# Kernel tuning notes

Hardware: AMD Instinct MI355X
Metric: run time of the kernel (lower is better)

The kernel has to match this reference:

```python
import jax, jax.numpy as jnp
import numpy as np

NUM_HEAD = 16
HEAD_DIM = 64
SEQ, BATCH, DMODEL = 2048, 2, 1024


def setup_inputs() -> dict:
    key = jax.random.key(0)
    ks = jax.random.split(key, 6)
    xavier = lambda k, shp: jax.random.uniform(
        k, shp, jnp.float32, -1.0, 1.0) * np.sqrt(6.0 / (shp[0] + shp[1]))
    query = jax.random.normal(ks[0], (SEQ, BATCH, DMODEL), jnp.float32)
    q_w = xavier(ks[1], (DMODEL, DMODEL))
    k_w = xavier(ks[2], (DMODEL, DMODEL))
    v_w = xavier(ks[3], (DMODEL, DMODEL))
    out_w = xavier(ks[4], (DMODEL, DMODEL))
    zeros = jnp.zeros((DMODEL,), jnp.float32)
    # causal mask: True = masked out (key position after query position)
    causal = jnp.triu(jnp.ones((SEQ, SEQ), bool), k=1)
    attn_mask = jnp.broadcast_to(causal, (BATCH, SEQ, SEQ))
    return {
        "query": query,
        "q_w": q_w, "q_b": zeros,
        "k_w": k_w, "k_b": zeros,
        "v_w": v_w, "v_b": zeros,
        "out_w": out_w, "out_b": zeros,
        "attn_mask": attn_mask,
    }


def reference(query, q_w, q_b, k_w, k_b, v_w, v_b, out_w, out_b, attn_mask):
    S, B, _ = query.shape
    H, Dh = NUM_HEAD, HEAD_DIM
    scale = 1.0 / np.sqrt(Dh)
    # self-attention: key = value = query
    q = (query @ q_w.T + q_b).reshape(S, B, H, Dh)
    k = (query @ k_w.T + k_b).reshape(S, B, H, Dh)
    v = (query @ v_w.T + v_b).reshape(S, B, H, Dh)
    # scores: [B, H, S(query), S(key)]
    scores = jnp.einsum('sbhd,tbhd->bhst', q, k) * scale
    scores = jnp.where(attn_mask[:, None, :, :], -jnp.inf, scores)
    attn = jax.nn.softmax(scores, axis=-1)
    # context: [S, B, H, Dh] -> [S, B, H*Dh]
    ctx = jnp.einsum('bhst,tbhd->sbhd', attn, v).reshape(S, B, H * Dh)
    return ctx @ out_w.T + out_b
```

## Files before the change

kernel.cpp:

```cpp
#include <hip/hip_runtime.h>
#include <hip/hip_bf16.h>

typedef __bf16 bf16;
typedef __attribute__((ext_vector_type(2))) __bf16 bf16x2;
typedef __attribute__((ext_vector_type(4))) __bf16 bf16x4;
typedef __attribute__((ext_vector_type(8))) __bf16 bf16x8;
typedef __attribute__((ext_vector_type(4))) float f32x4;

static_assert(sizeof(bf16x8) == 16, "bf16x8 must be 16B");

#define S_LEN 2048
#define BATCH_N 2
#define DM 1024
#define NHEAD 16
#define HDIM 64
#define LOG2E 1.44269504088896f

__device__ __forceinline__ void async_cp16(const void* g, void* l) {
    __builtin_amdgcn_global_load_lds(
        (const __attribute__((address_space(1))) void*)g,
        (__attribute__((address_space(3))) void*)l, 16, 0, 0);
}

__global__ __launch_bounds__(256)
void cvt_all(const float* __restrict__ q,
             const float* __restrict__ w0, const float* __restrict__ w1,
             const float* __restrict__ w2, const float* __restrict__ w3,
             bf16* __restrict__ Xb,
             bf16* __restrict__ W0, bf16* __restrict__ W1,
             bf16* __restrict__ W2, bf16* __restrict__ W3) {
    const int blk = blockIdx.x;
    const float* src;
    bf16* dst;
    size_t base;
    if (blk < 2048) {
        src = q; dst = Xb; base = (size_t)blk * 2048;
    } else {
        const int w = (blk - 2048) >> 9;
        const int r = (blk - 2048) & 511;
        base = (size_t)r * 2048;
        src = (w == 0) ? w0 : (w == 1) ? w1 : (w == 2) ? w2 : w3;
        dst = (w == 0) ? W0 : (w == 1) ? W1 : (w == 2) ? W2 : W3;
    }
    const size_t i = base + (size_t)threadIdx.x * 8;
    const f32x4 a = *(const f32x4*)(src + i);
    const f32x4 b = *(const f32x4*)(src + i + 4);
    bf16x8 r8;
    r8[0] = (bf16)a[0]; r8[1] = (bf16)a[1]; r8[2] = (bf16)a[2]; r8[3] = (bf16)a[3];
    r8[4] = (bf16)b[0]; r8[5] = (bf16)b[1]; r8[6] = (bf16)b[2]; r8[7] = (bf16)b[3];
    *(bf16x8*)(dst + i) = r8;
}

__device__ __forceinline__ void gemm_tile64(const bf16* __restrict__ A,
                                            const bf16* __restrict__ W,
                                            int row0, int col0, int Kdim,
                                            f32x4 acc[2][4]) {
    __shared__ bf16 As[64 * 32];
    __shared__ bf16 Bs[128 * 32];
    const int tid  = threadIdx.x;
    const int lane = tid & 63;
    const int wv   = tid >> 6;
    const int wr = wv >> 1, wc = wv & 1;
    const int qr = lane & 15, quad = lane >> 4;

    const int srow = wv * 16 + (lane >> 2);
    const int scol = (lane & 3) * 8;
    const bf16* Ap  = A + (size_t)(row0 + srow) * Kdim + scol;
    const bf16* Wp0 = W + (size_t)(col0 + srow) * Kdim + scol;
    const bf16* Wp1 = W + (size_t)(col0 + 64 + srow) * Kdim + scol;
    bf16* lA  = As + wv * 512;
    bf16* lB0 = Bs + wv * 512;
    bf16* lB1 = Bs + 64 * 32 + wv * 512;

    const f32x4 fzero = {0.f, 0.f, 0.f, 0.f};
    #pragma unroll
    for (int mi = 0; mi < 2; ++mi)
        #pragma unroll
        for (int ni = 0; ni < 4; ++ni)
            acc[mi][ni] = fzero;

    for (int k0 = 0; k0 < Kdim; k0 += 32) {
        __syncthreads();
        async_cp16(Ap + k0, lA);
        async_cp16(Wp0 + k0, lB0);
        async_cp16(Wp1 + k0, lB1);
        __syncthreads();

        bf16x8 af[2], bfr[4];
        #pragma unroll
        for (int mi = 0; mi < 2; ++mi)
            af[mi] = *(const bf16x8*)(As + (wr * 32 + mi * 16 + qr) * 32 + quad * 8);
        #pragma unroll
        for (int ni = 0; ni < 4; ++ni)
            bfr[ni] = *(const bf16x8*)(Bs + (wc * 64 + ni * 16 + qr) * 32 + quad * 8);
        #pragma unroll
        for (int mi = 0; mi < 2; ++mi)
            #pragma unroll
            for (int ni = 0; ni < 4; ++ni)
                acc[mi][ni] = __builtin_amdgcn_mfma_f32_16x16x32_bf16(
                    af[mi], bfr[ni], acc[mi][ni], 0, 0, 0);
    }
}

__global__ __launch_bounds__(256)
void qkv_kernel(const bf16* __restrict__ X,
                const bf16* __restrict__ Wq, const float* __restrict__ bq,
                const bf16* __restrict__ Wk, const float* __restrict__ bk,
                const bf16* __restrict__ Wv, const float* __restrict__ bv,
                bf16* __restrict__ Q, bf16* __restrict__ Kt, bf16* __restrict__ Vt) {
    const int mat  = blockIdx.z;
    const bf16*  W    = (mat == 0) ? Wq : (mat == 1) ? Wk : Wv;
    const float* bias = (mat == 0) ? bq : (mat == 1) ? bk : bv;
    const int col0 = blockIdx.x * 128;
    const int row0 = blockIdx.y * 64;

    f32x4 acc[2][4];
    gemm_tile64(X, W, row0, col0, DM, acc);

    const int lane = threadIdx.x & 63;
    const int wave = threadIdx.x >> 6;
    const int wr = wave >> 1, wc = wave & 1;
    const int qr = lane & 15, quad = lane >> 4;

    #pragma unroll
    for (int ni = 0; ni < 4; ++ni) {
        const int n  = col0 + wc * 64 + ni * 16 + qr;
        const float bn = bias[n];
        const int h = n >> 6, dh = n & 63;
        #pragma unroll
        for (int mi = 0; mi < 2; ++mi) {
            const int i0 = row0 + wr * 32 + mi * 16 + quad * 4;
            const float v0 = acc[mi][ni][0] + bn;
            const float v1 = acc[mi][ni][1] + bn;
            const float v2 = acc[mi][ni][2] + bn;
            const float v3 = acc[mi][ni][3] + bn;
            if (mat == 2) {
                const int s0 = i0 >> 1;
                bf16x2 e0 = {(bf16)v0, (bf16)v2};
                bf16x2 e1 = {(bf16)v1, (bf16)v3};
                *(bf16x2*)(Vt + ((size_t)h * HDIM + dh) * S_LEN + s0) = e0;
                *(bf16x2*)(Vt + ((size_t)(NHEAD + h) * HDIM + dh) * S_LEN + s0) = e1;
            } else {
                #pragma unroll
                for (int r = 0; r < 4; ++r) {
                    const int i = i0 + r;
                    const int s = i >> 1, b = i & 1;
                    const float v = (r == 0) ? v0 : (r == 1) ? v1 : (r == 2) ? v2 : v3;
                    if (mat == 0) {
                        Q[((size_t)(b * NHEAD + h) * S_LEN + s) * HDIM + dh] =
                            (bf16)(v * (0.125f * LOG2E));
                    } else {
                        Kt[((size_t)(b * NHEAD + h) * S_LEN + s) * HDIM + dh] = (bf16)v;
                    }
                }
            }
        }
    }
}

#define PLD 40
#define PT  640
#define WAVE_P (8*PT)
#define RSTRIDE 36

#define MFMA(a, b, c) __builtin_amdgcn_mfma_f32_16x16x32_bf16(a, b, c, 0, 0, 0)
#define EX(x) __builtin_amdgcn_exp2f(x)

#define QK_TILE(j) \
    f32x4 sA##j = MFMA(k0, qlo##j, fzero); sA##j = MFMA(k1, qhi##j, sA##j); \
    f32x4 sB##j = MFMA(k2, qlo##j, fzero); sB##j = MFMA(k3, qhi##j, sB##j);

#define SFULL(j) do { \
    const float e0 = EX(sA##j[0]), e1 = EX(sA##j[1]), e2 = EX(sA##j[2]), e3 = EX(sA##j[3]); \
    const float f0 = EX(sB##j[0]), f1 = EX(sB##j[1]), f2 = EX(sB##j[2]), f3 = EX(sB##j[3]); \
    l##j += (e0 + e1 + e2 + e3) + (f0 + f1 + f2 + f3); \
    bf16x4 wa = {(bf16)e0, (bf16)e1, (bf16)e2, (bf16)e3}; \
    bf16x4 wb = {(bf16)f0, (bf16)f1, (bf16)f2, (bf16)f3}; \
    *(bf16x4*)(PB + (j) * PT + qr * PLD + quad * 4)      = wa; \
    *(bf16x4*)(PB + (j) * PT + qr * PLD + 16 + quad * 4) = wb; \
} while (0)

#define SMASK(j) do { \
    const int qrow = qb0 + 16 * (j) + qr; \
    const int ka = t * 32 + quad * 4; \
    const float e0 = (ka + 0  <= qrow) ? EX(sA##j[0]) : 0.f; \
    const float e1 = (ka + 1  <= qrow) ? EX(sA##j[1]) : 0.f; \
    const float e2 = (ka + 2  <= qrow) ? EX(sA##j[2]) : 0.f; \
    const float e3 = (ka + 3  <= qrow) ? EX(sA##j[3]) : 0.f; \
    const float f0 = (ka + 16 <= qrow) ? EX(sB##j[0]) : 0.f; \
    const float f1 = (ka + 17 <= qrow) ? EX(sB##j[1]) : 0.f; \
    const float f2 = (ka + 18 <= qrow) ? EX(sB##j[2]) : 0.f; \
    const float f3 = (ka + 19 <= qrow) ? EX(sB##j[3]) : 0.f; \
    l##j += (e0 + e1 + e2 + e3) + (f0 + f1 + f2 + f3); \
    bf16x4 wa = {(bf16)e0, (bf16)e1, (bf16)e2, (bf16)e3}; \
    bf16x4 wb = {(bf16)f0, (bf16)f1, (bf16)f2, (bf16)f3}; \
    *(bf16x4*)(PB + (j) * PT + qr * PLD + quad * 4)      = wa; \
    *(bf16x4*)(PB + (j) * PT + qr * PLD + 16 + quad * 4) = wb; \
} while (0)

__global__ __launch_bounds__(256)
void attn_kernel(const bf16* __restrict__ Q, const bf16* __restrict__ K,
                 const bf16* __restrict__ Vt, bf16* __restrict__ ctx) {
    __shared__ __align__(16) char smem[40960];
    const int lane = threadIdx.x & 63;
    const int wave = threadIdx.x >> 6;
    const int qr = lane & 15, quad = lane >> 4;
    const int bh = blockIdx.y;
    const int b = bh >> 4, h = bh & 15;
    const int qb0 = ((int)gridDim.x - 1 - (int)blockIdx.x) * 64;
    const int tdiag = qb0 >> 5;
    const int tmax  = tdiag + 1;

    const bf16* Qb = Q  + (size_t)bh * S_LEN * HDIM;
    const bf16* Kb = K  + (size_t)bh * S_LEN * HDIM;
    const bf16* Vb = Vt + (size_t)bh * HDIM * S_LEN;

    const bf16x8 qlo0 = *(const bf16x8*)(Qb + (size_t)(qb0 + qr) * HDIM + quad * 8);
    const bf16x8 qhi0 = *(const bf16x8*)(Qb + (size_t)(qb0 + qr) * HDIM + quad * 8 + 32);
    const bf16x8 qlo1 = *(const bf16x8*)(Qb + (size_t)(qb0 + 16 + qr) * HDIM + quad * 8);
    const bf16x8 qhi1 = *(const bf16x8*)(Qb + (size_t)(qb0 + 16 + qr) * HDIM + quad * 8 + 32);
    const bf16x8 qlo2 = *(const bf16x8*)(Qb + (size_t)(qb0 + 32 + qr) * HDIM + quad * 8);
    const bf16x8 qhi2 = *(const bf16x8*)(Qb + (size_t)(qb0 + 32 + qr) * HDIM + quad * 8 + 32);
    const bf16x8 qlo3 = *(const bf16x8*)(Qb + (size_t)(qb0 + 48 + qr) * HDIM + quad * 8);
    const bf16x8 qhi3 = *(const bf16x8*)(Qb + (size_t)(qb0 + 48 + qr) * HDIM + quad * 8 + 32);

    const f32x4 fzero = {0.f, 0.f, 0.f, 0.f};
    f32x4 o0_0 = fzero, o0_1 = fzero, o0_2 = fzero, o0_3 = fzero;
    f32x4 o1_0 = fzero, o1_1 = fzero, o1_2 = fzero, o1_3 = fzero;
    f32x4 o2_0 = fzero, o2_1 = fzero, o2_2 = fzero, o2_3 = fzero;
    f32x4 o3_0 = fzero, o3_1 = fzero, o3_2 = fzero, o3_3 = fzero;
    float l0 = 0.f, l1 = 0.f, l2 = 0.f, l3 = 0.f;
    bf16* Pw = (bf16*)smem + wave * WAVE_P;

    for (int t = wave, c = 0; t <= tmax; t += 4, ++c) {
        const bf16* kp = Kb + ((size_t)t * 32 + qr) * HDIM + quad * 8;
        const bf16x8 k0 = *(const bf16x8*)(kp);
        const bf16x8 k1 = *(const bf16x8*)(kp + 32);
        const bf16x8 k2 = *(const bf16x8*)(kp + 16 * HDIM);
        const bf16x8 k3 = *(const bf16x8*)(kp + 16 * HDIM + 32);
        const bf16* vp = Vb + (size_t)qr * S_LEN + t * 32 + quad * 8;
        const bf16x8 v0 = *(const bf16x8*)(vp);
        const bf16x8 v1 = *(const bf16x8*)(vp + 16 * S_LEN);
        const bf16x8 v2 = *(const bf16x8*)(vp + 32 * S_LEN);
        const bf16x8 v3 = *(const bf16x8*)(vp + 48 * S_LEN);
        bf16* PB = Pw + (c & 1) * (4 * PT);

        if (t < tdiag) {
            QK_TILE(0); SFULL(0);
            QK_TILE(1); SFULL(1);
            QK_TILE(2); SFULL(2);
            QK_TILE(3); SFULL(3);
        } else {
            QK_TILE(0); SMASK(0);
            QK_TILE(1); SMASK(1);
            QK_TILE(2); SMASK(2);
            QK_TILE(3); SMASK(3);
        }

        const bf16x8 pf0 = *(const bf16x8*)(PB + 0 * PT + qr * PLD + quad * 8);
        const bf16x8 pf1 = *(const bf16x8*)(PB + 1 * PT + qr * PLD + quad * 8);
        const bf16x8 pf2 = *(const bf16x8*)(PB + 2 * PT + qr * PLD + quad * 8);
        const bf16x8 pf3 = *(const bf16x8*)(PB + 3 * PT + qr * PLD + quad * 8);
        o0_0 = MFMA(v0, pf0, o0_0); o0_1 = MFMA(v1, pf0, o0_1);
        o0_2 = MFMA(v2, pf0, o0_2); o0_3 = MFMA(v3, pf0, o0_3);
        o1_0 = MFMA(v0, pf1, o1_0); o1_1 = MFMA(v1, pf1, o1_1);
        o1_2 = MFMA(v2, pf1, o1_2); o1_3 = MFMA(v3, pf1, o1_3);
        o2_0 = MFMA(v0, pf2, o2_0); o2_1 = MFMA(v1, pf2, o2_1);
        o2_2 = MFMA(v2, pf2, o2_2); o2_3 = MFMA(v3, pf2, o2_3);
        o3_0 = MFMA(v0, pf3, o3_0); o3_1 = MFMA(v1, pf3, o3_1);
        o3_2 = MFMA(v2, pf3, o3_2); o3_3 = MFMA(v3, pf3, o3_3);
    }

    __syncthreads();
    float* red = (float*)smem;
    if (wave != 0) {
        float* rp = red + ((size_t)(wave - 1) * 64 + lane) * RSTRIDE;
        *(f32x4*)(rp +  0) = o0_0; *(f32x4*)(rp +  4) = o0_1;
        *(f32x4*)(rp +  8) = o0_2; *(f32x4*)(rp + 12) = o0_3;
        *(f32x4*)(rp + 16) = o1_0; *(f32x4*)(rp + 20) = o1_1;
        *(f32x4*)(rp + 24) = o1_2; *(f32x4*)(rp + 28) = o1_3;
        rp[32] = l0; rp[33] = l1;
    }
    __syncthreads();
    if (wave == 0) {
        #pragma unroll
        for (int w = 0; w < 3; ++w) {
            const float* rp = red + ((size_t)w * 64 + lane) * RSTRIDE;
            o0_0 += *(const f32x4*)(rp +  0); o0_1 += *(const f32x4*)(rp +  4);
            o0_2 += *(const f32x4*)(rp +  8); o0_3 += *(const f32x4*)(rp + 12);
            o1_0 += *(const f32x4*)(rp + 16); o1_1 += *(const f32x4*)(rp + 20);
            o1_2 += *(const f32x4*)(rp + 24); o1_3 += *(const f32x4*)(rp + 28);
            l0 += rp[32]; l1 += rp[33];
        }
    }
    __syncthreads();
    if (wave != 0) {
        float* rp = red + ((size_t)(wave - 1) * 64 + lane) * RSTRIDE;
        *(f32x4*)(rp +  0) = o2_0; *(f32x4*)(rp +  4) = o2_1;
        *(f32x4*)(rp +  8) = o2_2; *(f32x4*)(rp + 12) = o2_3;
        *(f32x4*)(rp + 16) = o3_0; *(f32x4*)(rp + 20) = o3_1;
        *(f32x4*)(rp + 24) = o3_2; *(f32x4*)(rp + 28) = o3_3;
        rp[32] = l2; rp[33] = l3;
    }
    __syncthreads();
    if (wave == 0) {
        #pragma unroll
        for (int w = 0; w < 3; ++w) {
            const float* rp = red + ((size_t)w * 64 + lane) * RSTRIDE;
            o2_0 += *(const f32x4*)(rp +  0); o2_1 += *(const f32x4*)(rp +  4);
            o2_2 += *(const f32x4*)(rp +  8); o2_3 += *(const f32x4*)(rp + 12);
            o3_0 += *(const f32x4*)(rp + 16); o3_1 += *(const f32x4*)(rp + 20);
            o3_2 += *(const f32x4*)(rp + 24); o3_3 += *(const f32x4*)(rp + 28);
            l2 += rp[32]; l3 += rp[33];
        }
        l0 += __shfl_xor(l0, 16); l0 += __shfl_xor(l0, 32);
        l1 += __shfl_xor(l1, 16); l1 += __shfl_xor(l1, 32);
        l2 += __shfl_xor(l2, 16); l2 += __shfl_xor(l2, 32);
        l3 += __shfl_xor(l3, 16); l3 += __shfl_xor(l3, 32);
        const float inv0 = 1.f / l0, inv1 = 1.f / l1;
        const float inv2 = 1.f / l2, inv3 = 1.f / l3;

        #define OWRITE(ov, ni_, qrow_, inv_) do { \
            bf16x4 cc = {(bf16)(ov[0] * (inv_)), (bf16)(ov[1] * (inv_)), \
                         (bf16)(ov[2] * (inv_)), (bf16)(ov[3] * (inv_))}; \
            *(bf16x4*)(ctx + (size_t)((qrow_) * BATCH_N + b) * DM \
                       + h * 64 + (ni_) * 16 + quad * 4) = cc; \
        } while (0)
        OWRITE(o0_0, 0, qb0 + qr, inv0);      OWRITE(o0_1, 1, qb0 + qr, inv0);
        OWRITE(o0_2, 2, qb0 + qr, inv0);      OWRITE(o0_3, 3, qb0 + qr, inv0);
        OWRITE(o1_0, 0, qb0 + 16 + qr, inv1); OWRITE(o1_1, 1, qb0 + 16 + qr, inv1);
        OWRITE(o1_2, 2, qb0 + 16 + qr, inv1); OWRITE(o1_3, 3, qb0 + 16 + qr, inv1);
        OWRITE(o2_0, 0, qb0 + 32 + qr, inv2); OWRITE(o2_1, 1, qb0 + 32 + qr, inv2);
        OWRITE(o2_2, 2, qb0 + 32 + qr, inv2); OWRITE(o2_3, 3, qb0 + 32 + qr, inv2);
        OWRITE(o3_0, 0, qb0 + 48 + qr, inv3); OWRITE(o3_1, 1, qb0 + 48 + qr, inv3);
        OWRITE(o3_2, 2, qb0 + 48 + qr, inv3); OWRITE(o3_3, 3, qb0 + 48 + qr, inv3);
        #undef OWRITE
    }
}

__global__ __launch_bounds__(256)
void proj_kernel(const bf16* __restrict__ X, const bf16* __restrict__ W,
                 const float* __restrict__ bias, float* __restrict__ out) {
    const int col0 = blockIdx.x * 128;
    const int row0 = blockIdx.y * 64;
    f32x4 acc[2][4];
    gemm_tile64(X, W, row0, col0, DM, acc);

    const int lane = threadIdx.x & 63;
    const int wave = threadIdx.x >> 6;
    const int wr = wave >> 1, wc = wave & 1;
    const int qr = lane & 15, quad = lane >> 4;

    #pragma unroll
    for (int ni = 0; ni < 4; ++ni) {
        const int n = col0 + wc * 64 + ni * 16 + qr;
        const float bn = bias[n];
        #pragma unroll
        for (int mi = 0; mi < 2; ++mi) {
            #pragma unroll
            for (int r = 0; r < 4; ++r) {
                const int i = row0 + wr * 32 + mi * 16 + quad * 4 + r;
                out[(size_t)i * DM + n] = acc[mi][ni][r] + bn;
            }
        }
    }
}

extern "C" void kernel_launch(void* const* d_in, const int* in_sizes, int n_in,
                              void* d_out, int out_size, void* d_ws, size_t ws_size,
                              hipStream_t stream) {
    (void)in_sizes; (void)n_in; (void)out_size; (void)ws_size;
    const float* query = (const float*)d_in[0];
    const float* q_w   = (const float*)d_in[1];
    const float* q_b   = (const float*)d_in[2];
    const float* k_w   = (const float*)d_in[3];
    const float* k_b   = (const float*)d_in[4];
    const float* v_w   = (const float*)d_in[5];
    const float* v_b   = (const float*)d_in[6];
    const float* out_w = (const float*)d_in[7];
    const float* out_b = (const float*)d_in[8];

    char* ws = (char*)d_ws;
    bf16* Xb  = (bf16*)(ws);
    bf16* Wqb = (bf16*)(ws + ((size_t)8  << 20));
    bf16* Wkb = (bf16*)(ws + ((size_t)10 << 20));
    bf16* Wvb = (bf16*)(ws + ((size_t)12 << 20));
    bf16* Wob = (bf16*)(ws + ((size_t)14 << 20));
    bf16* Qb  = (bf16*)(ws + ((size_t)16 << 20));
    bf16* Kb  = (bf16*)(ws + ((size_t)24 << 20));
    bf16* Vt  = (bf16*)(ws + ((size_t)32 << 20));
    bf16* ctx = (bf16*)(ws + ((size_t)40 << 20));
    float* out = (float*)d_out;

    dim3 blk(256);
    cvt_all<<<dim3(2048 + 4 * 512), blk, 0, stream>>>(
        query, q_w, k_w, v_w, out_w, Xb, Wqb, Wkb, Wvb, Wob);

    qkv_kernel<<<dim3(DM / 128, (S_LEN * BATCH_N) / 64, 3), blk, 0, stream>>>(
        Xb, Wqb, q_b, Wkb, k_b, Wvb, v_b, Qb, Kb, Vt);
    attn_kernel<<<dim3(S_LEN / 64, BATCH_N * NHEAD), blk, 0, stream>>>(
        Qb, Kb, Vt, ctx);
    proj_kernel<<<dim3(DM / 128, (S_LEN * BATCH_N) / 64), blk, 0, stream>>>(
        ctx, Wob, out_b, out);
}
```

Before: 247.3 us.

## Split attention over key chunks with a reduce pass, enlarge GEMM tiles to 128x128

Attention is split into up to four key-range chunks per 64-row query block, giving 80 blocks per head instead of 32, which balances causal work across CUs. Unnormalized partial outputs and row sums are written to workspace, and a new reduce kernel sums them and normalizes. The QKV and output-projection GEMMs move from 64x128 to 128x128 tiles for more reuse per block. The per-wave P buffer loses its double buffering, which lowers shared memory use. The cost is an extra launch and global traffic for the partials, and partials are rounded to bf16 before they are summed.

```diff
diff --git a/kernel.cpp b/kernel.cpp
--- a/kernel.cpp
+++ b/kernel.cpp
@@ -51,11 +51,11 @@
     *(bf16x8*)(dst + i) = r8;
 }
 
-__device__ __forceinline__ void gemm_tile64(const bf16* __restrict__ A,
-                                            const bf16* __restrict__ W,
-                                            int row0, int col0, int Kdim,
-                                            f32x4 acc[2][4]) {
-    __shared__ bf16 As[64 * 32];
+__device__ __forceinline__ void gemm_tile(const bf16* __restrict__ A,
+                                          const bf16* __restrict__ W,
+                                          int row0, int col0, int Kdim,
+                                          f32x4 acc[4][4]) {
+    __shared__ bf16 As[128 * 32];
     __shared__ bf16 Bs[128 * 32];
     const int tid  = threadIdx.x;
     const int lane = tid & 63;
@@ -65,36 +65,37 @@
 
     const int srow = wv * 16 + (lane >> 2);
     const int scol = (lane & 3) * 8;
-    const bf16* Ap  = A + (size_t)(row0 + srow) * Kdim + scol;
-    const bf16* Wp0 = W + (size_t)(col0 + srow) * Kdim + scol;
-    const bf16* Wp1 = W + (size_t)(col0 + 64 + srow) * Kdim + scol;
-    bf16* lA  = As + wv * 512;
+    const bf16* Ap = A + (size_t)(row0 + srow) * Kdim + scol;
+    const bf16* Wp = W + (size_t)(col0 + srow) * Kdim + scol;
+    bf16* lA0 = As + wv * 512;
+    bf16* lA1 = As + 64 * 32 + wv * 512;
     bf16* lB0 = Bs + wv * 512;
     bf16* lB1 = Bs + 64 * 32 + wv * 512;
 
     const f32x4 fzero = {0.f, 0.f, 0.f, 0.f};
     #pragma unroll
-    for (int mi = 0; mi < 2; ++mi)
+    for (int mi = 0; mi < 4; ++mi)
         #pragma unroll
         for (int ni = 0; ni < 4; ++ni)
             acc[mi][ni] = fzero;
 
     for (int k0 = 0; k0 < Kdim; k0 += 32) {
         __syncthreads();
-        async_cp16(Ap + k0, lA);
-        async_cp16(Wp0 + k0, lB0);
-        async_cp16(Wp1 + k0, lB1);
+        async_cp16(Ap + k0, lA0);
+        async_cp16(Ap + (size_t)64 * Kdim + k0, lA1);
+        async_cp16(Wp + k0, lB0);
+        async_cp16(Wp + (size_t)64 * Kdim + k0, lB1);
         __syncthreads();
 
-        bf16x8 af[2], bfr[4];
-        #pragma unroll
-        for (int mi = 0; mi < 2; ++mi)
-            af[mi] = *(const bf16x8*)(As + (wr * 32 + mi * 16 + qr) * 32 + quad * 8);
+        bf16x8 af[4], bfr[4];
+        #pragma unroll
+        for (int mi = 0; mi < 4; ++mi)
+            af[mi] = *(const bf16x8*)(As + (wr * 64 + mi * 16 + qr) * 32 + quad * 8);
         #pragma unroll
         for (int ni = 0; ni < 4; ++ni)
             bfr[ni] = *(const bf16x8*)(Bs + (wc * 64 + ni * 16 + qr) * 32 + quad * 8);
         #pragma unroll
-        for (int mi = 0; mi < 2; ++mi)
+        for (int mi = 0; mi < 4; ++mi)
             #pragma unroll
             for (int ni = 0; ni < 4; ++ni)
                 acc[mi][ni] = __builtin_amdgcn_mfma_f32_16x16x32_bf16(
@@ -112,10 +113,10 @@
     const bf16*  W    = (mat == 0) ? Wq : (mat == 1) ? Wk : Wv;
     const float* bias = (mat == 0) ? bq : (mat == 1) ? bk : bv;
     const int col0 = blockIdx.x * 128;
-    const int row0 = blockIdx.y * 64;
-
-    f32x4 acc[2][4];
-    gemm_tile64(X, W, row0, col0, DM, acc);
+    const int row0 = blockIdx.y * 128;
+
+    f32x4 acc[4][4];
+    gemm_tile(X, W, row0, col0, DM, acc);
 
     const int lane = threadIdx.x & 63;
     const int wave = threadIdx.x >> 6;
@@ -128,8 +129,8 @@
         const float bn = bias[n];
         const int h = n >> 6, dh = n & 63;
         #pragma unroll
-        for (int mi = 0; mi < 2; ++mi) {
-            const int i0 = row0 + wr * 32 + mi * 16 + quad * 4;
+        for (int mi = 0; mi < 4; ++mi) {
+            const int i0 = row0 + wr * 64 + mi * 16 + quad * 4;
             const float v0 = acc[mi][ni][0] + bn;
             const float v1 = acc[mi][ni][1] + bn;
             const float v2 = acc[mi][ni][2] + bn;
@@ -160,7 +161,6 @@
 
 #define PLD 40
 #define PT  640
-#define WAVE_P (8*PT)
 #define RSTRIDE 36
 
 #define MFMA(a, b, c) __builtin_amdgcn_mfma_f32_16x16x32_bf16(a, b, c, 0, 0, 0)
@@ -176,8 +176,8 @@
     l##j += (e0 + e1 + e2 + e3) + (f0 + f1 + f2 + f3); \
     bf16x4 wa = {(bf16)e0, (bf16)e1, (bf16)e2, (bf16)e3}; \
     bf16x4 wb = {(bf16)f0, (bf16)f1, (bf16)f2, (bf16)f3}; \
-    *(bf16x4*)(PB + (j) * PT + qr * PLD + quad * 4)      = wa; \
-    *(bf16x4*)(PB + (j) * PT + qr * PLD + 16 + quad * 4) = wb; \
+    *(bf16x4*)(Pw + (j) * PT + qr * PLD + quad * 4)      = wa; \
+    *(bf16x4*)(Pw + (j) * PT + qr * PLD + 16 + quad * 4) = wb; \
 } while (0)
 
 #define SMASK(j) do { \
@@ -194,22 +194,30 @@
     l##j += (e0 + e1 + e2 + e3) + (f0 + f1 + f2 + f3); \
     bf16x4 wa = {(bf16)e0, (bf16)e1, (bf16)e2, (bf16)e3}; \
     bf16x4 wb = {(bf16)f0, (bf16)f1, (bf16)f2, (bf16)f3}; \
-    *(bf16x4*)(PB + (j) * PT + qr * PLD + quad * 4)      = wa; \
-    *(bf16x4*)(PB + (j) * PT + qr * PLD + 16 + quad * 4) = wb; \
+    *(bf16x4*)(Pw + (j) * PT + qr * PLD + quad * 4)      = wa; \
+    *(bf16x4*)(Pw + (j) * PT + qr * PLD + 16 + quad * 4) = wb; \
 } while (0)
 
 __global__ __launch_bounds__(256)
-void attn_kernel(const bf16* __restrict__ Q, const bf16* __restrict__ K,
-                 const bf16* __restrict__ Vt, bf16* __restrict__ ctx) {
-    __shared__ __align__(16) char smem[40960];
+void attn_part(const bf16* __restrict__ Q, const bf16* __restrict__ K,
+               const bf16* __restrict__ Vt,
+               bf16* __restrict__ Pout, float* __restrict__ Pl) {
+    __shared__ __align__(16) char smem[27648];
     const int lane = threadIdx.x & 63;
     const int wave = threadIdx.x >> 6;
     const int qr = lane & 15, quad = lane >> 4;
     const int bh = blockIdx.y;
-    const int b = bh >> 4, h = bh & 15;
-    const int qb0 = ((int)gridDim.x - 1 - (int)blockIdx.x) * 64;
-    const int tdiag = qb0 >> 5;
-    const int tmax  = tdiag + 1;
+    const int f  = blockIdx.x;
+    int qb, c;
+    if (f < 8)       { qb = f;                c = 0; }
+    else if (f < 24) { qb = 8 + ((f - 8) >> 1);  c = (f - 8) & 1; }
+    else if (f < 48) { qb = 16 + (f - 24) / 3;   c = (f - 24) % 3; }
+    else             { qb = 24 + ((f - 48) >> 2); c = (f - 48) & 3; }
+    const int qb0    = qb * 64;
+    const int tdiag  = qb * 2;
+    const int ntiles = 2 * qb + 2;
+    const int t0     = c * 16;
+    const int tend   = min(t0 + 16, ntiles);
 
     const bf16* Qb = Q  + (size_t)bh * S_LEN * HDIM;
     const bf16* Kb = K  + (size_t)bh * S_LEN * HDIM;
@@ -230,9 +238,9 @@
     f32x4 o2_0 = fzero, o2_1 = fzero, o2_2 = fzero, o2_3 = fzero;
     f32x4 o3_0 = fzero, o3_1 = fzero, o3_2 = fzero, o3_3 = fzero;
     float l0 = 0.f, l1 = 0.f, l2 = 0.f, l3 = 0.f;
-    bf16* Pw = (bf16*)smem + wave * WAVE_P;
-
-    for (int t = wave, c = 0; t <= tmax; t += 4, ++c) {
+    bf16* Pw = (bf16*)smem + wave * (4 * PT);
+
+    for (int t = t0 + wave; t < tend; t += 4) {
         const bf16* kp = Kb + ((size_t)t * 32 + qr) * HDIM + quad * 8;
         const bf16x8 k0 = *(const bf16x8*)(kp);
         const bf16x8 k1 = *(const bf16x8*)(kp + 32);
@@ -243,7 +251,6 @@
         const bf16x8 v1 = *(const bf16x8*)(vp + 16 * S_LEN);
         const bf16x8 v2 = *(const bf16x8*)(vp + 32 * S_LEN);
         const bf16x8 v3 = *(const bf16x8*)(vp + 48 * S_LEN);
-        bf16* PB = Pw + (c & 1) * (4 * PT);
 
         if (t < tdiag) {
             QK_TILE(0); SFULL(0);
@@ -257,10 +264,10 @@
             QK_TILE(3); SMASK(3);
         }
 
-        const bf16x8 pf0 = *(const bf16x8*)(PB + 0 * PT + qr * PLD + quad * 8);
-        const bf16x8 pf1 = *(const bf16x8*)(PB + 1 * PT + qr * PLD + quad * 8);
-        const bf16x8 pf2 = *(const bf16x8*)(PB + 2 * PT + qr * PLD + quad * 8);
-        const bf16x8 pf3 = *(const bf16x8*)(PB + 3 * PT + qr * PLD + quad * 8);
+        const bf16x8 pf0 = *(const bf16x8*)(Pw + 0 * PT + qr * PLD + quad * 8);
+        const bf16x8 pf1 = *(const bf16x8*)(Pw + 1 * PT + qr * PLD + quad * 8);
+        const bf16x8 pf2 = *(const bf16x8*)(Pw + 2 * PT + qr * PLD + quad * 8);
+        const bf16x8 pf3 = *(const bf16x8*)(Pw + 3 * PT + qr * PLD + quad * 8);
         o0_0 = MFMA(v0, pf0, o0_0); o0_1 = MFMA(v1, pf0, o0_1);
         o0_2 = MFMA(v2, pf0, o0_2); o0_3 = MFMA(v3, pf0, o0_3);
         o1_0 = MFMA(v0, pf1, o1_0); o1_1 = MFMA(v1, pf1, o1_1);
@@ -317,34 +324,67 @@
         l1 += __shfl_xor(l1, 16); l1 += __shfl_xor(l1, 32);
         l2 += __shfl_xor(l2, 16); l2 += __shfl_xor(l2, 32);
         l3 += __shfl_xor(l3, 16); l3 += __shfl_xor(l3, 32);
-        const float inv0 = 1.f / l0, inv1 = 1.f / l1;
-        const float inv2 = 1.f / l2, inv3 = 1.f / l3;
-
-        #define OWRITE(ov, ni_, qrow_, inv_) do { \
-            bf16x4 cc = {(bf16)(ov[0] * (inv_)), (bf16)(ov[1] * (inv_)), \
-                         (bf16)(ov[2] * (inv_)), (bf16)(ov[3] * (inv_))}; \
-            *(bf16x4*)(ctx + (size_t)((qrow_) * BATCH_N + b) * DM \
-                       + h * 64 + (ni_) * 16 + quad * 4) = cc; \
+
+        const size_t sidx = ((size_t)bh * 32 + qb) * 4 + c;
+        bf16* po = Pout + sidx * 4096;
+        float* pl = Pl + sidx * 64;
+        #define PWRITE(ov, ni_, jrow_) do { \
+            bf16x4 cc = {(bf16)ov[0], (bf16)ov[1], (bf16)ov[2], (bf16)ov[3]}; \
+            *(bf16x4*)(po + (size_t)((jrow_) * 16 + qr) * 64 + (ni_) * 16 + quad * 4) = cc; \
         } while (0)
-        OWRITE(o0_0, 0, qb0 + qr, inv0);      OWRITE(o0_1, 1, qb0 + qr, inv0);
-        OWRITE(o0_2, 2, qb0 + qr, inv0);      OWRITE(o0_3, 3, qb0 + qr, inv0);
-        OWRITE(o1_0, 0, qb0 + 16 + qr, inv1); OWRITE(o1_1, 1, qb0 + 16 + qr, inv1);
-        OWRITE(o1_2, 2, qb0 + 16 + qr, inv1); OWRITE(o1_3, 3, qb0 + 16 + qr, inv1);
-        OWRITE(o2_0, 0, qb0 + 32 + qr, inv2); OWRITE(o2_1, 1, qb0 + 32 + qr, inv2);
-        OWRITE(o2_2, 2, qb0 + 32 + qr, inv2); OWRITE(o2_3, 3, qb0 + 32 + qr, inv2);
-        OWRITE(o3_0, 0, qb0 + 48 + qr, inv3); OWRITE(o3_1, 1, qb0 + 48 + qr, inv3);
-        OWRITE(o3_2, 2, qb0 + 48 + qr, inv3); OWRITE(o3_3, 3, qb0 + 48 + qr, inv3);
-        #undef OWRITE
-    }
+        PWRITE(o0_0, 0, 0); PWRITE(o0_1, 1, 0); PWRITE(o0_2, 2, 0); PWRITE(o0_3, 3, 0);
+        PWRITE(o1_0, 0, 1); PWRITE(o1_1, 1, 1); PWRITE(o1_2, 2, 1); PWRITE(o1_3, 3, 1);
+        PWRITE(o2_0, 0, 2); PWRITE(o2_1, 1, 2); PWRITE(o2_2, 2, 2); PWRITE(o2_3, 3, 2);
+        PWRITE(o3_0, 0, 3); PWRITE(o3_1, 1, 3); PWRITE(o3_2, 2, 3); PWRITE(o3_3, 3, 3);
+        #undef PWRITE
+        if (quad == 0) {
+            pl[qr]      = l0;
+            pl[16 + qr] = l1;
+            pl[32 + qr] = l2;
+            pl[48 + qr] = l3;
+        }
+    }
+}
+
+__global__ __launch_bounds__(256)
+void attn_reduce(const bf16* __restrict__ Pout, const float* __restrict__ Pl,
+                 bf16* __restrict__ ctx) {
+    const int qb = blockIdx.x, bh = blockIdx.y;
+    const int b = bh >> 4, h = bh & 15;
+    const int nc = (qb < 8) ? 1 : (qb < 16) ? 2 : (qb < 24) ? 3 : 4;
+    const int tid = threadIdx.x;
+    const int row = tid >> 2;
+    const int dg  = (tid & 3) * 16;
+    const size_t base = ((size_t)bh * 32 + qb) * 4;
+
+    float acc[16];
+    #pragma unroll
+    for (int i = 0; i < 16; ++i) acc[i] = 0.f;
+    float lsum = 0.f;
+    for (int cc = 0; cc < nc; ++cc) {
+        const bf16* po = Pout + (base + cc) * 4096 + (size_t)row * 64 + dg;
+        const bf16x8 x0 = *(const bf16x8*)(po);
+        const bf16x8 x1 = *(const bf16x8*)(po + 8);
+        #pragma unroll
+        for (int i = 0; i < 8; ++i) { acc[i] += (float)x0[i]; acc[8 + i] += (float)x1[i]; }
+        lsum += Pl[(base + cc) * 64 + row];
+    }
+    const float inv = 1.f / lsum;
+    bf16x8 y0, y1;
+    #pragma unroll
+    for (int i = 0; i < 8; ++i) { y0[i] = (bf16)(acc[i] * inv); y1[i] = (bf16)(acc[8 + i] * inv); }
+    bf16* cp = ctx + ((size_t)(qb * 64 + row) * BATCH_N + b) * DM + h * 64 + dg;
+    *(bf16x8*)cp = y0;
+    *(bf16x8*)(cp + 8) = y1;
 }
 
 __global__ __launch_bounds__(256)
 void proj_kernel(const bf16* __restrict__ X, const bf16* __restrict__ W,
                  const float* __restrict__ bias, float* __restrict__ out) {
     const int col0 = blockIdx.x * 128;
-    const int row0 = blockIdx.y * 64;
-    f32x4 acc[2][4];
-    gemm_tile64(X, W, row0, col0, DM, acc);
+    const int row0 = blockIdx.y * 128;
+    f32x4 acc[4][4];
+    gemm_tile(X, W, row0, col0, DM, acc);
 
     const int lane = threadIdx.x & 63;
     const int wave = threadIdx.x >> 6;
@@ -356,10 +396,10 @@
         const int n = col0 + wc * 64 + ni * 16 + qr;
         const float bn = bias[n];
         #pragma unroll
-        for (int mi = 0; mi < 2; ++mi) {
+        for (int mi = 0; mi < 4; ++mi) {
             #pragma unroll
             for (int r = 0; r < 4; ++r) {
-                const int i = row0 + wr * 32 + mi * 16 + quad * 4 + r;
+                const int i = row0 + wr * 64 + mi * 16 + quad * 4 + r;
                 out[(size_t)i * DM + n] = acc[mi][ni][r] + bn;
             }
         }
@@ -381,25 +421,27 @@
     const float* out_b = (const float*)d_in[8];
 
     char* ws = (char*)d_ws;
-    bf16* Xb  = (bf16*)(ws);
-    bf16* Wqb = (bf16*)(ws + ((size_t)8  << 20));
-    bf16* Wkb = (bf16*)(ws + ((size_t)10 << 20));
-    bf16* Wvb = (bf16*)(ws + ((size_t)12 << 20));
-    bf16* Wob = (bf16*)(ws + ((size_t)14 << 20));
-    bf16* Qb  = (bf16*)(ws + ((size_t)16 << 20));
-    bf16* Kb  = (bf16*)(ws + ((size_t)24 << 20));
-    bf16* Vt  = (bf16*)(ws + ((size_t)32 << 20));
-    bf16* ctx = (bf16*)(ws + ((size_t)40 << 20));
-    float* out = (float*)d_out;
+    bf16*  Qb   = (bf16*)(ws);
+    bf16*  Kb   = (bf16*)(ws + ((size_t)8  << 20));
+    bf16*  Vt   = (bf16*)(ws + ((size_t)16 << 20));
+    bf16*  ctx  = (bf16*)(ws + ((size_t)24 << 20));
+    bf16*  Wob  = (bf16*)(ws + ((size_t)32 << 20));
+    bf16*  Xb   = (bf16*)(ws + ((size_t)34 << 20));
+    bf16*  Wqb  = (bf16*)(ws + ((size_t)42 << 20));
+    bf16*  Wkb  = (bf16*)(ws + ((size_t)44 << 20));
+    bf16*  Wvb  = (bf16*)(ws + ((size_t)46 << 20));
+    bf16*  Pout = (bf16*)(ws + ((size_t)34 << 20));
+    float* Pl   = (float*)(ws + ((size_t)66 << 20));
+    float* out  = (float*)d_out;
 
     dim3 blk(256);
     cvt_all<<<dim3(2048 + 4 * 512), blk, 0, stream>>>(
         query, q_w, k_w, v_w, out_w, Xb, Wqb, Wkb, Wvb, Wob);
 
-    qkv_kernel<<<dim3(DM / 128, (S_LEN * BATCH_N) / 64, 3), blk, 0, stream>>>(
+    qkv_kernel<<<dim3(DM / 128, (S_LEN * BATCH_N) / 128, 3), blk, 0, stream>>>(
         Xb, Wqb, q_b, Wkb, k_b, Wvb, v_b, Qb, Kb, Vt);
-    attn_kernel<<<dim3(S_LEN / 64, BATCH_N * NHEAD), blk, 0, stream>>>(
-        Qb, Kb, Vt, ctx);
-    proj_kernel<<<dim3(DM / 128, (S_LEN * BATCH_N) / 64), blk, 0, stream>>>(
+    attn_part<<<dim3(80, BATCH_N * NHEAD), blk, 0, stream>>>(Qb, Kb, Vt, Pout, Pl);
+    attn_reduce<<<dim3(S_LEN / 64, BATCH_N * NHEAD), blk, 0, stream>>>(Pout, Pl, ctx);
+    proj_kernel<<<dim3(DM / 128, (S_LEN * BATCH_N) / 128), blk, 0, stream>>>(
         ctx, Wob, out_b, out);
 }
```

After: 236.0 us. 1.05x faster.
